# Kernel optimization log

Hardware: AMD Instinct MI355X
Metric: run time of the kernel (lower is better)

The kernel has to match this reference:

```python
import jax, jax.numpy as jnp
import numpy as np

N_EXPERTS = 8
D_IN = 512
D_OUT = 512


def setup_inputs() -> dict:
    key = jax.random.key(0)
    k1, k2, k3, k4 = jax.random.split(key, 4)
    B, N = 16, 4096
    z = jax.random.randint(k1, (B, N), 0, N_EXPERTS, dtype=jnp.int64 if jax.config.jax_enable_x64 else jnp.int32)
    x = jax.random.normal(k2, (B, N, D_IN), dtype=jnp.float32)
    # Expert parameters: map_list[e] modeled as Linear(D_IN, D_OUT)
    W = jax.random.normal(k3, (N_EXPERTS, D_IN, D_OUT), dtype=jnp.float32) * (1.0 / np.sqrt(D_IN))
    b = jax.random.normal(k4, (N_EXPERTS, D_OUT), dtype=jnp.float32) * 0.01
    return {"z": z, "x": x, "W": W, "b": b}


def reference(z, x, W, b):
    B, N = z.shape
    z_flat = z.reshape(-1)                 # [T]
    x_flat = x.reshape(-1, x.shape[-1])    # [T, D_in]
    T = z_flat.shape[0]
    y = jnp.zeros((T, D_OUT), dtype=x.dtype)
    # Dense equivalent of mask-gather -> expert apply -> masked scatter.
    # Tokens with id == -1 (or any id not hit) stay zero, matching the torch code.
    for e in range(N_EXPERTS):
        mask = (z_flat == e)[:, None]      # [T, 1]
        y_e = x_flat @ W[e] + b[e]         # [T, D_out]
        y = jnp.where(mask, y_e, y)
    y = y.reshape(B, N, D_OUT)
    return (z, y)
```

## Files before the change

### kernel.cpp

```cpp
#include <hip/hip_runtime.h>
#include <stdint.h>

#define NEXP 8
#define DD   512
#define BM   128
#define BN   128

typedef short s16x8 __attribute__((ext_vector_type(8)));
typedef float f32x4 __attribute__((ext_vector_type(4)));

static __device__ __forceinline__ unsigned short f2bf(float f) {
    union { float f; unsigned u; } v; v.f = f;
    unsigned r = v.u + 0x7FFFu + ((v.u >> 16) & 1u);
    return (unsigned short)(r >> 16);
}


__global__ void hist_kernel(const int* __restrict__ z, int* __restrict__ counts, int T) {
    __shared__ int lc[NEXP];
    int tid = threadIdx.x;
    if (tid < NEXP) lc[tid] = 0;
    __syncthreads();
    int t = blockIdx.x * blockDim.x + tid;
    if (t < T) atomicAdd(&lc[z[t]], 1);
    __syncthreads();
    if (tid < NEXP) atomicAdd(&counts[tid], lc[tid]);
}

__global__ void scan_kernel(const int* __restrict__ counts, int* __restrict__ cursors,
                            int4* __restrict__ table, int max_tiles) {
    __shared__ int off[NEXP + 1];
    __shared__ int tb[NEXP + 1];
    int tid = threadIdx.x;
    if (tid == 0) {
        int o = 0, tbs = 0;
        for (int e = 0; e < NEXP; e++) {
            off[e] = o; tb[e] = tbs;
            cursors[e] = o;
            int c = counts[e];
            o += c;
            tbs += (c + BM - 1) / BM;
        }
        off[NEXP] = o; tb[NEXP] = tbs;
    }
    __syncthreads();
    for (int idx = tid; idx < max_tiles; idx += blockDim.x) {
        int4 ent; ent.x = -1; ent.y = 0; ent.z = 0; ent.w = 0;
#pragma unroll
        for (int e = 0; e < NEXP; e++) {
            if (idx >= tb[e] && idx < tb[e + 1]) {
                int r = (idx - tb[e]) * BM;
                ent.x = e; ent.y = off[e] + r; ent.z = (off[e + 1] - off[e]) - r;
            }
        }
        table[idx] = ent;
    }
}

__global__ void scatter_kernel(const int* __restrict__ z, int* __restrict__ cursors,
                               int* __restrict__ token_index, float* __restrict__ zout, int T) {
    __shared__ int lc[NEXP];
    __shared__ int lbase[NEXP];
    int tid = threadIdx.x;
    if (tid < NEXP) lc[tid] = 0;
    __syncthreads();
    int t = blockIdx.x * blockDim.x + tid;
    int e = 0, rank = 0;
    if (t < T) {
        e = z[t];
        rank = atomicAdd(&lc[e], 1);
        zout[t] = (float)e;
    }
    __syncthreads();
    if (tid < NEXP) lbase[tid] = atomicAdd(&cursors[tid], lc[tid]);
    __syncthreads();
    if (t < T) token_index[lbase[e] + rank] = t;
}

__global__ __launch_bounds__(256) void gather_kernel(const float* __restrict__ x,
                                                     const int* __restrict__ token_index,
                                                     unsigned short* __restrict__ xg, int T) {
    int i = blockIdx.x * 4 + (threadIdx.x >> 6);
    if (i >= T) return;
    int lane = threadIdx.x & 63;
    int t = token_index[i];
    const float4* src = (const float4*)(x + (size_t)t * DD) + lane * 2;
    float4 v0 = src[0], v1 = src[1];
    uint4 p;
    p.x = (unsigned)f2bf(v0.x) | ((unsigned)f2bf(v0.y) << 16);
    p.y = (unsigned)f2bf(v0.z) | ((unsigned)f2bf(v0.w) << 16);
    p.z = (unsigned)f2bf(v1.x) | ((unsigned)f2bf(v1.y) << 16);
    p.w = (unsigned)f2bf(v1.z) | ((unsigned)f2bf(v1.w) << 16);
    *(uint4*)(xg + (size_t)i * DD + lane * 8) = p;
}

__global__ void convw_kernel(const float* __restrict__ W, unsigned short* __restrict__ Wt) {
    __shared__ float tile[32][33];
    int e = blockIdx.z, k0 = blockIdx.x * 32, n0 = blockIdx.y * 32;
    int tid = threadIdx.x;
    const float* We = W + (size_t)e * DD * DD;
    unsigned short* WtE = Wt + (size_t)e * DD * DD;
    int c = tid & 31, r0 = tid >> 5;
#pragma unroll
    for (int i = 0; i < 4; i++) {
        int kr = r0 + 8 * i;
        tile[kr][c] = We[(size_t)(k0 + kr) * DD + n0 + c];
    }
    __syncthreads();
#pragma unroll
    for (int i = 0; i < 4; i++) {
        int nr = r0 + 8 * i;
        WtE[(size_t)(n0 + nr) * DD + k0 + c] = f2bf(tile[c][nr]);
    }
}


__global__ __launch_bounds__(256) void gemm2_kernel(
    const unsigned short* __restrict__ xg,
    const unsigned short* __restrict__ Wt,
    const float* __restrict__ bias,
    const int* __restrict__ token_index,
    const int4* __restrict__ table,
    float* __restrict__ y)
{
    int4 te = table[blockIdx.x];
    int e = te.x;
    if (e < 0) return;
    const int base = te.y;
    const int rows_valid = te.z < BM ? te.z : BM;
    const int n0 = blockIdx.y * BN;

    __shared__ unsigned short Als[BM * 64];
    __shared__ unsigned short Bls[BN * 64];

    const int tid  = threadIdx.x;
    const int lane = tid & 63;
    const int wave = tid >> 6;
    const int wm = (wave & 1) * 64;
    const int wn = (wave >> 1) * 64;

    int srow[4], schunk[4];
#pragma unroll
    for (int q = 0; q < 4; q++) {
        int s = wave * 256 + q * 64 + lane;
        srow[q]   = s >> 3;
        schunk[q] = (s & 7) ^ ((s >> 3) & 7);
    }

    const unsigned short* WtE = Wt + (size_t)e * DD * DD;

    f32x4 acc[4][4];
#pragma unroll
    for (int i = 0; i < 4; i++)
#pragma unroll
        for (int j = 0; j < 4; j++) acc[i][j] = (f32x4){0.f, 0.f, 0.f, 0.f};

    const int quad = lane >> 4;
    const int lrow = lane & 15;

    for (int k0 = 0; k0 < DD; k0 += 64) {
        __syncthreads();
#pragma unroll
        for (int q = 0; q < 4; q++) {
            const int r = srow[q], c = schunk[q];
            const unsigned short* ga = xg + (size_t)(base + r) * DD + k0 + c * 8;
            const unsigned short* gb = WtE + (size_t)(n0 + r) * DD + k0 + c * 8;
            unsigned short* la = &Als[(size_t)(wave * 256 + q * 64) * 8];
            unsigned short* lb = &Bls[(size_t)(wave * 256 + q * 64) * 8];
            __builtin_amdgcn_global_load_lds((const __attribute__((address_space(1))) void*)ga,
                                             (__attribute__((address_space(3))) void*)la, 16, 0, 0);
            __builtin_amdgcn_global_load_lds((const __attribute__((address_space(1))) void*)gb,
                                             (__attribute__((address_space(3))) void*)lb, 16, 0, 0);
        }
        __syncthreads();

#pragma unroll
        for (int ks = 0; ks < 2; ks++) {
            s16x8 af[4], bq[4];
#pragma unroll
            for (int i = 0; i < 4; i++) {
                int r = wm + i * 16 + lrow;
                af[i] = *(const s16x8*)(&Als[r * 64 + (((quad + 4 * ks) ^ (r & 7)) * 8)]);
            }
#pragma unroll
            for (int j = 0; j < 4; j++) {
                int r = wn + j * 16 + lrow;
                bq[j] = *(const s16x8*)(&Bls[r * 64 + (((quad + 4 * ks) ^ (r & 7)) * 8)]);
            }
#pragma unroll
            for (int i = 0; i < 4; i++)
#pragma unroll
                for (int j = 0; j < 4; j++)
                    acc[i][j] = __builtin_amdgcn_mfma_f32_16x16x32_bf16(af[i], bq[j], acc[i][j], 0, 0, 0);
        }
    }

    const int lcol = lane & 15;
    float bv[4];
#pragma unroll
    for (int j = 0; j < 4; j++) bv[j] = bias[e * DD + n0 + wn + j * 16 + lcol];
#pragma unroll
    for (int i = 0; i < 4; i++) {
#pragma unroll
        for (int reg = 0; reg < 4; reg++) {
            int r = wm + i * 16 + quad * 4 + reg;
            if (r < rows_valid) {
                int t = token_index[base + r];
                float* yr = y + (size_t)t * DD + n0 + wn + lcol;
#pragma unroll
                for (int j = 0; j < 4; j++)
                    yr[j * 16] = acc[i][j][reg] + bv[j];
            }
        }
    }
}


__global__ __launch_bounds__(256) void gemm_kernel(
    const float* __restrict__ x, const unsigned short* __restrict__ Wt,
    const float* __restrict__ bias, const int* __restrict__ token_index,
    const int4* __restrict__ table, float* __restrict__ y)
{
    int4 te = table[blockIdx.x];
    int e = te.x;
    if (e < 0) return;
    int base = te.y;
    int rows_valid = te.z < BM ? te.z : BM;
    int n0 = blockIdx.y * BN;

    __shared__ unsigned short Als[BM * 40];
    __shared__ unsigned short Bls[BN * 40];

    const int tid  = threadIdx.x;
    const int lane = tid & 63;
    const int wave = tid >> 6;
    const int wm = (wave & 1) * 64;
    const int wn = (wave >> 1) * 64;

    const int a_q  = tid & 7;
    const int a_r0 = tid >> 3;
    int tok[4];
#pragma unroll
    for (int i = 0; i < 4; i++) {
        int r = a_r0 + 32 * i;
        int rr = (r < rows_valid) ? r : 0;
        tok[i] = token_index[base + rr];
    }
    const int b_c  = tid & 3;
    const int b_n0 = tid >> 2;
    const unsigned short* WtE = Wt + (size_t)e * DD * DD;

    f32x4 acc[4][4];
#pragma unroll
    for (int i = 0; i < 4; i++)
#pragma unroll
        for (int j = 0; j < 4; j++) acc[i][j] = (f32x4){0.f, 0.f, 0.f, 0.f};

    const int quad = lane >> 4;
    const int lrow = lane & 15;

    for (int k0 = 0; k0 < DD; k0 += 32) {
        __syncthreads();
#pragma unroll
        for (int i = 0; i < 4; i++) {
            int r = a_r0 + 32 * i;
            const float4 v = *(const float4*)(x + (size_t)tok[i] * DD + k0 + a_q * 4);
            unsigned u0 = (unsigned)f2bf(v.x) | ((unsigned)f2bf(v.y) << 16);
            unsigned u1 = (unsigned)f2bf(v.z) | ((unsigned)f2bf(v.w) << 16);
            uint2 p; p.x = u0; p.y = u1;
            *(uint2*)(&Als[r * 40 + a_q * 4]) = p;
        }
#pragma unroll
        for (int i = 0; i < 2; i++) {
            int n = b_n0 + 64 * i;
            uint4 v = *(const uint4*)(WtE + (size_t)(n0 + n) * DD + k0 + b_c * 8);
            *(uint4*)(&Bls[n * 40 + b_c * 8]) = v;
        }
        __syncthreads();

        s16x8 af[4], bq[4];
#pragma unroll
        for (int i = 0; i < 4; i++)
            af[i] = *(const s16x8*)(&Als[(wm + i * 16 + lrow) * 40 + quad * 8]);
#pragma unroll
        for (int j = 0; j < 4; j++)
            bq[j] = *(const s16x8*)(&Bls[(wn + j * 16 + lrow) * 40 + quad * 8]);
#pragma unroll
        for (int i = 0; i < 4; i++)
#pragma unroll
            for (int j = 0; j < 4; j++)
                acc[i][j] = __builtin_amdgcn_mfma_f32_16x16x32_bf16(af[i], bq[j], acc[i][j], 0, 0, 0);
    }

    const int lcol = lane & 15;
    float bv[4];
#pragma unroll
    for (int j = 0; j < 4; j++) bv[j] = bias[e * DD + n0 + wn + j * 16 + lcol];
#pragma unroll
    for (int i = 0; i < 4; i++) {
#pragma unroll
        for (int reg = 0; reg < 4; reg++) {
            int r = wm + i * 16 + quad * 4 + reg;
            if (r < rows_valid) {
                int t = token_index[base + r];
                float* yr = y + (size_t)t * DD + n0 + wn + lcol;
#pragma unroll
                for (int j = 0; j < 4; j++)
                    yr[j * 16] = acc[i][j][reg] + bv[j];
            }
        }
    }
}


extern "C" void kernel_launch(void* const* d_in, const int* in_sizes, int n_in,
                              void* d_out, int out_size, void* d_ws, size_t ws_size,
                              hipStream_t stream) {
    const int*   z = (const int*)d_in[0];
    const float* x = (const float*)d_in[1];
    const float* W = (const float*)d_in[2];
    const float* b = (const float*)d_in[3];
    const int T = in_sizes[0];

    float* zout = (float*)d_out;
    float* y    = (float*)d_out + T;

    char* ws = (char*)d_ws;
    int*  counts      = (int*)ws;
    int*  cursors     = (int*)(ws + 64);
    int4* table       = (int4*)(ws + 256);
    int*  token_index = (int*)(ws + 16640);
    unsigned short* Wt = (unsigned short*)(ws + 278784);
    unsigned short* xg = (unsigned short*)(ws + 4473344);

    const int max_tiles = T / BM + NEXP;
    const size_t need = 4473344 + (size_t)T * DD * 2 + 131072;

    hipMemsetAsync(ws, 0, 64, stream);
    hist_kernel<<<(T + 255) / 256, 256, 0, stream>>>(z, counts, T);
    convw_kernel<<<dim3(DD / 32, DD / 32, NEXP), 256, 0, stream>>>(W, Wt);
    scan_kernel<<<1, 256, 0, stream>>>(counts, cursors, table, max_tiles);
    scatter_kernel<<<(T + 255) / 256, 256, 0, stream>>>(z, cursors, token_index, zout, T);

    if (ws_size >= need) {
        gather_kernel<<<(T + 3) / 4, 256, 0, stream>>>(x, token_index, xg, T);
        gemm2_kernel<<<dim3(max_tiles, DD / BN), 256, 0, stream>>>(xg, Wt, b, token_index, table, y);
    } else {
        gemm_kernel<<<dim3(max_tiles, DD / BN), 256, 0, stream>>>(x, Wt, b, token_index, table, y);
    }
}
```

Before: 336.3 us.

## Fuse token gather and bf16 conversion into full-width expert GEMM

```diff
diff --git a/kernel.cpp b/kernel.cpp
--- a/kernel.cpp
+++ b/kernel.cpp
@@ -3,8 +3,8 @@
 
 #define NEXP 8
 #define DD   512
-#define BM   128
-#define BN   128
+#define BM   64
+#define BN   512
 
 typedef short s16x8 __attribute__((ext_vector_type(8)));
 typedef float f32x4 __attribute__((ext_vector_type(4)));
@@ -77,23 +77,6 @@
     if (t < T) token_index[lbase[e] + rank] = t;
 }
 
-__global__ __launch_bounds__(256) void gather_kernel(const float* __restrict__ x,
-                                                     const int* __restrict__ token_index,
-                                                     unsigned short* __restrict__ xg, int T) {
-    int i = blockIdx.x * 4 + (threadIdx.x >> 6);
-    if (i >= T) return;
-    int lane = threadIdx.x & 63;
-    int t = token_index[i];
-    const float4* src = (const float4*)(x + (size_t)t * DD) + lane * 2;
-    float4 v0 = src[0], v1 = src[1];
-    uint4 p;
-    p.x = (unsigned)f2bf(v0.x) | ((unsigned)f2bf(v0.y) << 16);
-    p.y = (unsigned)f2bf(v0.z) | ((unsigned)f2bf(v0.w) << 16);
-    p.z = (unsigned)f2bf(v1.x) | ((unsigned)f2bf(v1.y) << 16);
-    p.w = (unsigned)f2bf(v1.z) | ((unsigned)f2bf(v1.w) << 16);
-    *(uint4*)(xg + (size_t)i * DD + lane * 8) = p;
-}
-
 __global__ void convw_kernel(const float* __restrict__ W, unsigned short* __restrict__ Wt) {
     __shared__ float tile[32][33];
     int e = blockIdx.z, k0 = blockIdx.x * 32, n0 = blockIdx.y * 32;
@@ -115,8 +98,8 @@
 }
 
 
-__global__ __launch_bounds__(256) void gemm2_kernel(
-    const unsigned short* __restrict__ xg,
+__global__ __launch_bounds__(512, 4) void gemm3_kernel(
+    const float* __restrict__ x,
     const unsigned short* __restrict__ Wt,
     const float* __restrict__ bias,
     const int* __restrict__ token_index,
@@ -124,11 +107,10 @@
     float* __restrict__ y)
 {
     int4 te = table[blockIdx.x];
-    int e = te.x;
+    const int e = te.x;
     if (e < 0) return;
     const int base = te.y;
     const int rows_valid = te.z < BM ? te.z : BM;
-    const int n0 = blockIdx.y * BN;
 
     __shared__ unsigned short Als[BM * 64];
     __shared__ unsigned short Bls[BN * 64];
@@ -136,18 +118,18 @@
     const int tid  = threadIdx.x;
     const int lane = tid & 63;
     const int wave = tid >> 6;
-    const int wm = (wave & 1) * 64;
-    const int wn = (wave >> 1) * 64;
-
-    int srow[4], schunk[4];
-#pragma unroll
-    for (int q = 0; q < 4; q++) {
-        int s = wave * 256 + q * 64 + lane;
-        srow[q]   = s >> 3;
-        schunk[q] = (s & 7) ^ ((s >> 3) & 7);
-    }
-
-    const unsigned short* WtE = Wt + (size_t)e * DD * DD;
+    const int wn   = wave * 64;
+
+    const int ra  = tid >> 3;
+    const int ca  = tid & 7;
+    const int gca = ca ^ (ra & 7);
+
+    const int rr  = (ra < rows_valid) ? ra : 0;
+    const int tok = token_index[base + rr];
+    const float* asrc = x + (size_t)tok * DD + gca * 8;
+
+    const unsigned short* WtE  = Wt + (size_t)e * DD * DD;
+    const unsigned short* bsrc = WtE + (size_t)ra * DD + gca * 8;
 
     f32x4 acc[4][4];
 #pragma unroll
@@ -158,20 +140,28 @@
     const int quad = lane >> 4;
     const int lrow = lane & 15;
 
+    float4 av0 = *(const float4*)(asrc);
+    float4 av1 = *(const float4*)(asrc + 4);
+
     for (int k0 = 0; k0 < DD; k0 += 64) {
         __syncthreads();
-#pragma unroll
-        for (int q = 0; q < 4; q++) {
-            const int r = srow[q], c = schunk[q];
-            const unsigned short* ga = xg + (size_t)(base + r) * DD + k0 + c * 8;
-            const unsigned short* gb = WtE + (size_t)(n0 + r) * DD + k0 + c * 8;
-            unsigned short* la = &Als[(size_t)(wave * 256 + q * 64) * 8];
-            unsigned short* lb = &Bls[(size_t)(wave * 256 + q * 64) * 8];
-            __builtin_amdgcn_global_load_lds((const __attribute__((address_space(1))) void*)ga,
-                                             (__attribute__((address_space(3))) void*)la, 16, 0, 0);
+        uint4 p;
+        p.x = (unsigned)f2bf(av0.x) | ((unsigned)f2bf(av0.y) << 16);
+        p.y = (unsigned)f2bf(av0.z) | ((unsigned)f2bf(av0.w) << 16);
+        p.z = (unsigned)f2bf(av1.x) | ((unsigned)f2bf(av1.y) << 16);
+        p.w = (unsigned)f2bf(av1.z) | ((unsigned)f2bf(av1.w) << 16);
+        *(uint4*)(&Als[tid * 8]) = p;
+#pragma unroll
+        for (int j = 0; j < 8; j++) {
+            const unsigned short* gb = bsrc + (size_t)j * 64 * DD + k0;
+            unsigned short* lb = &Bls[(size_t)(tid + j * 512) * 8];
             __builtin_amdgcn_global_load_lds((const __attribute__((address_space(1))) void*)gb,
                                              (__attribute__((address_space(3))) void*)lb, 16, 0, 0);
         }
+        if (k0 + 64 < DD) {
+            av0 = *(const float4*)(asrc + k0 + 64);
+            av1 = *(const float4*)(asrc + k0 + 68);
+        }
         __syncthreads();
 
 #pragma unroll
@@ -179,13 +169,13 @@
             s16x8 af[4], bq[4];
 #pragma unroll
             for (int i = 0; i < 4; i++) {
-                int r = wm + i * 16 + lrow;
+                int r = i * 16 + lrow;
                 af[i] = *(const s16x8*)(&Als[r * 64 + (((quad + 4 * ks) ^ (r & 7)) * 8)]);
             }
 #pragma unroll
             for (int j = 0; j < 4; j++) {
-                int r = wn + j * 16 + lrow;
-                bq[j] = *(const s16x8*)(&Bls[r * 64 + (((quad + 4 * ks) ^ (r & 7)) * 8)]);
+                int n = wn + j * 16 + lrow;
+                bq[j] = *(const s16x8*)(&Bls[n * 64 + (((quad + 4 * ks) ^ (n & 7)) * 8)]);
             }
 #pragma unroll
             for (int i = 0; i < 4; i++)
@@ -198,112 +188,15 @@
     const int lcol = lane & 15;
     float bv[4];
 #pragma unroll
-    for (int j = 0; j < 4; j++) bv[j] = bias[e * DD + n0 + wn + j * 16 + lcol];
+    for (int j = 0; j < 4; j++) bv[j] = bias[e * DD + wn + j * 16 + lcol];
 #pragma unroll
     for (int i = 0; i < 4; i++) {
 #pragma unroll
         for (int reg = 0; reg < 4; reg++) {
-            int r = wm + i * 16 + quad * 4 + reg;
+            int r = i * 16 + quad * 4 + reg;
             if (r < rows_valid) {
                 int t = token_index[base + r];
-                float* yr = y + (size_t)t * DD + n0 + wn + lcol;
-#pragma unroll
-                for (int j = 0; j < 4; j++)
-                    yr[j * 16] = acc[i][j][reg] + bv[j];
-            }
-        }
-    }
-}
-
-
-__global__ __launch_bounds__(256) void gemm_kernel(
-    const float* __restrict__ x, const unsigned short* __restrict__ Wt,
-    const float* __restrict__ bias, const int* __restrict__ token_index,
-    const int4* __restrict__ table, float* __restrict__ y)
-{
-    int4 te = table[blockIdx.x];
-    int e = te.x;
-    if (e < 0) return;
-    int base = te.y;
-    int rows_valid = te.z < BM ? te.z : BM;
-    int n0 = blockIdx.y * BN;
-
-    __shared__ unsigned short Als[BM * 40];
-    __shared__ unsigned short Bls[BN * 40];
-
-    const int tid  = threadIdx.x;
-    const int lane = tid & 63;
-    const int wave = tid >> 6;
-    const int wm = (wave & 1) * 64;
-    const int wn = (wave >> 1) * 64;
-
-    const int a_q  = tid & 7;
-    const int a_r0 = tid >> 3;
-    int tok[4];
-#pragma unroll
-    for (int i = 0; i < 4; i++) {
-        int r = a_r0 + 32 * i;
-        int rr = (r < rows_valid) ? r : 0;
-        tok[i] = token_index[base + rr];
-    }
-    const int b_c  = tid & 3;
-    const int b_n0 = tid >> 2;
-    const unsigned short* WtE = Wt + (size_t)e * DD * DD;
-
-    f32x4 acc[4][4];
-#pragma unroll
-    for (int i = 0; i < 4; i++)
-#pragma unroll
-        for (int j = 0; j < 4; j++) acc[i][j] = (f32x4){0.f, 0.f, 0.f, 0.f};
-
-    const int quad = lane >> 4;
-    const int lrow = lane & 15;
-
-    for (int k0 = 0; k0 < DD; k0 += 32) {
-        __syncthreads();
-#pragma unroll
-        for (int i = 0; i < 4; i++) {
-            int r = a_r0 + 32 * i;
-            const float4 v = *(const float4*)(x + (size_t)tok[i] * DD + k0 + a_q * 4);
-            unsigned u0 = (unsigned)f2bf(v.x) | ((unsigned)f2bf(v.y) << 16);
-            unsigned u1 = (unsigned)f2bf(v.z) | ((unsigned)f2bf(v.w) << 16);
-            uint2 p; p.x = u0; p.y = u1;
-            *(uint2*)(&Als[r * 40 + a_q * 4]) = p;
-        }
-#pragma unroll
-        for (int i = 0; i < 2; i++) {
-            int n = b_n0 + 64 * i;
-            uint4 v = *(const uint4*)(WtE + (size_t)(n0 + n) * DD + k0 + b_c * 8);
-            *(uint4*)(&Bls[n * 40 + b_c * 8]) = v;
-        }
-        __syncthreads();
-
-        s16x8 af[4], bq[4];
-#pragma unroll
-        for (int i = 0; i < 4; i++)
-            af[i] = *(const s16x8*)(&Als[(wm + i * 16 + lrow) * 40 + quad * 8]);
-#pragma unroll
-        for (int j = 0; j < 4; j++)
-            bq[j] = *(const s16x8*)(&Bls[(wn + j * 16 + lrow) * 40 + quad * 8]);
-#pragma unroll
-        for (int i = 0; i < 4; i++)
-#pragma unroll
-            for (int j = 0; j < 4; j++)
-                acc[i][j] = __builtin_amdgcn_mfma_f32_16x16x32_bf16(af[i], bq[j], acc[i][j], 0, 0, 0);
-    }
-
-    const int lcol = lane & 15;
-    float bv[4];
-#pragma unroll
-    for (int j = 0; j < 4; j++) bv[j] = bias[e * DD + n0 + wn + j * 16 + lcol];
-#pragma unroll
-    for (int i = 0; i < 4; i++) {
-#pragma unroll
-        for (int reg = 0; reg < 4; reg++) {
-            int r = wm + i * 16 + quad * 4 + reg;
-            if (r < rows_valid) {
-                int t = token_index[base + r];
-                float* yr = y + (size_t)t * DD + n0 + wn + lcol;
+                float* yr = y + (size_t)t * DD + wn + lcol;
 #pragma unroll
                 for (int j = 0; j < 4; j++)
                     yr[j * 16] = acc[i][j][reg] + bv[j];
@@ -329,23 +222,15 @@
     int*  counts      = (int*)ws;
     int*  cursors     = (int*)(ws + 64);
     int4* table       = (int4*)(ws + 256);
-    int*  token_index = (int*)(ws + 16640);
-    unsigned short* Wt = (unsigned short*)(ws + 278784);
-    unsigned short* xg = (unsigned short*)(ws + 4473344);
+    int*  token_index = (int*)(ws + 17408);
+    unsigned short* Wt = (unsigned short*)(ws + 279552);
 
     const int max_tiles = T / BM + NEXP;
-    const size_t need = 4473344 + (size_t)T * DD * 2 + 131072;
 
     hipMemsetAsync(ws, 0, 64, stream);
     hist_kernel<<<(T + 255) / 256, 256, 0, stream>>>(z, counts, T);
     convw_kernel<<<dim3(DD / 32, DD / 32, NEXP), 256, 0, stream>>>(W, Wt);
     scan_kernel<<<1, 256, 0, stream>>>(counts, cursors, table, max_tiles);
     scatter_kernel<<<(T + 255) / 256, 256, 0, stream>>>(z, cursors, token_index, zout, T);
-
-    if (ws_size >= need) {
-        gather_kernel<<<(T + 3) / 4, 256, 0, stream>>>(x, token_index, xg, T);
-        gemm2_kernel<<<dim3(max_tiles, DD / BN), 256, 0, stream>>>(xg, Wt, b, token_index, table, y);
-    } else {
-        gemm_kernel<<<dim3(max_tiles, DD / BN), 256, 0, stream>>>(x, Wt, b, token_index, table, y);
-    }
-}
+    gemm3_kernel<<<dim3(max_tiles), 512, 0, stream>>>(x, Wt, b, token_index, table, y);
+}
```

After: 309.9 us. -7.9%, faster.
